# Kernel optimization log

Hardware: AMD Instinct MI355X
Metric: run time of the kernel (lower is better)

The kernel has to match this reference:

```python
import jax, jax.numpy as jnp
import numpy as np

D_MODEL = 1024
N_HEAD = 16


def setup_inputs() -> dict:
    key = jax.random.key(0)
    ks = jax.random.split(key, 9)
    d = D_MODEL
    s = 0.02
    return {
        "x": jax.random.normal(ks[0], (4, 2048, d), dtype=jnp.float32),
        "w_q": jax.random.normal(ks[1], (d, d), dtype=jnp.float32) * s,
        "b_q": jax.random.normal(ks[2], (d,), dtype=jnp.float32) * s,
        "w_k": jax.random.normal(ks[3], (d, d), dtype=jnp.float32) * s,
        "b_k": jax.random.normal(ks[4], (d,), dtype=jnp.float32) * s,
        "w_v": jax.random.normal(ks[5], (d, d), dtype=jnp.float32) * s,
        "b_v": jax.random.normal(ks[6], (d,), dtype=jnp.float32) * s,
        "w_o": jax.random.normal(ks[7], (d, d), dtype=jnp.float32) * s,
        "b_o": jax.random.normal(ks[8], (d,), dtype=jnp.float32) * s,
    }


def reference(x, w_q, b_q, w_k, b_k, w_v, b_v, w_o, b_o):
    B, S, D = x.shape
    H = N_HEAD
    dh = D // H

    def split(t):  # [B,S,D] -> [B,H,S,dh]
        return t.reshape(B, S, H, dh).transpose(0, 2, 1, 3)

    q = split(x @ w_q + b_q)
    k = split(x @ w_k + b_k)
    v = split(x @ w_v + b_v)

    scale = 1.0 / jnp.sqrt(jnp.float32(dh))
    score = jnp.einsum("bhqd,bhkd->bhqk", q, k) * scale
    score = jax.nn.softmax(score, axis=-1)
    out = jnp.einsum("bhqk,bhkd->bhqd", score, v)
    out = out.transpose(0, 2, 1, 3).reshape(B, S, D)
    return out @ w_o + b_o
```

## Files before the change

kernel.cpp:

```cpp
#include <hip/hip_runtime.h>


typedef __bf16 bf16x8 __attribute__((ext_vector_type(8)));
typedef float f32x4 __attribute__((ext_vector_type(4)));
typedef float f32x16 __attribute__((ext_vector_type(16)));
typedef unsigned short u16x8 __attribute__((ext_vector_type(8)));
typedef unsigned u32x4 __attribute__((ext_vector_type(4)));
typedef unsigned u32x2 __attribute__((ext_vector_type(2)));

#define SEQ 2048
#define DM 1024
#define NHEAD 16
#define MTOT 8192
#define QSCALE 0.18033688011112042f

__device__ __forceinline__ unsigned short f2bf(float f) {
  unsigned u = __builtin_bit_cast(unsigned, f);
  u += 0x7fffu + ((u >> 16) & 1u);
  return (unsigned short)(u >> 16);
}

__device__ __forceinline__ unsigned pkbf(float lo, float hi) {
  __bf16 a = (__bf16)lo, b = (__bf16)hi;
  return ((unsigned)__builtin_bit_cast(unsigned short, b) << 16) |
         __builtin_bit_cast(unsigned short, a);
}

__device__ __forceinline__ void async16(const void* g, void* l) {
  __builtin_amdgcn_global_load_lds(
      (const __attribute__((address_space(1))) void*)g,
      (__attribute__((address_space(3))) void*)l, 16, 0, 0);
}

template <bool CX>
__device__ __forceinline__ void exch(unsigned A, unsigned B, unsigned& fr0, unsigned& fr2) {
#if __has_builtin(__builtin_amdgcn_permlane32_swap)
  if constexpr (CX) {
    u32x2 r = __builtin_amdgcn_permlane32_swap(B, A, false, false);
    fr0 = r[1]; fr2 = r[0];
  } else {
    u32x2 r = __builtin_amdgcn_permlane32_swap(A, B, false, false);
    fr0 = r[0]; fr2 = r[1];
  }
#else
  int hi = (threadIdx.x & 63) >> 5;
  unsigned sA = (unsigned)__shfl_xor((int)A, 32);
  unsigned sB = (unsigned)__shfl_xor((int)B, 32);
  fr0 = hi ? sB : A;
  fr2 = hi ? B : sA;
#endif
}

__device__ __forceinline__ float halfsum(float rs) {
#if __has_builtin(__builtin_amdgcn_permlane32_swap)
  unsigned rb = __builtin_bit_cast(unsigned, rs);
  u32x2 rr = __builtin_amdgcn_permlane32_swap(rb, rb, false, false);
  return __builtin_bit_cast(float, rr[0]) + __builtin_bit_cast(float, rr[1]);
#else
  return rs + __shfl_xor(rs, 32);
#endif
}

__global__ __launch_bounds__(256) void k_cvt(const float* __restrict__ x,
                                             unsigned short* __restrict__ xb) {
  size_t i = ((size_t)blockIdx.x * 256 + threadIdx.x) * 8;
  float4 a = *(const float4*)(x + i);
  float4 b = *(const float4*)(x + i + 4);
  u16x8 o;
  o[0] = f2bf(a.x); o[1] = f2bf(a.y); o[2] = f2bf(a.z); o[3] = f2bf(a.w);
  o[4] = f2bf(b.x); o[5] = f2bf(b.y); o[6] = f2bf(b.z); o[7] = f2bf(b.w);
  *(u16x8*)(xb + i) = o;
}

__global__ __launch_bounds__(256) void k_wt(const float* __restrict__ w0, const float* __restrict__ w1,
                                            const float* __restrict__ w2, const float* __restrict__ w3,
                                            unsigned short* __restrict__ t0, unsigned short* __restrict__ t1,
                                            unsigned short* __restrict__ t2, unsigned short* __restrict__ t3) {
  __shared__ float t[64][65];
  int z = blockIdx.z;
  const float* w = z == 0 ? w0 : z == 1 ? w1 : z == 2 ? w2 : w3;
  unsigned short* wt = z == 0 ? t0 : z == 1 ? t1 : z == 2 ? t2 : t3;
  int nt = blockIdx.x, kt = blockIdx.y;
  int tx = threadIdx.x & 63, ty = threadIdx.x >> 6;
  for (int i = 0; i < 16; ++i) {
    int r = i * 4 + ty;
    t[r][tx] = w[(size_t)(kt * 64 + r) * DM + nt * 64 + tx];
  }
  __syncthreads();
  for (int i = 0; i < 16; ++i) {
    int r = i * 4 + ty;
    wt[(size_t)(nt * 64 + r) * DM + kt * 64 + tx] = f2bf(t[tx][r]);
  }
}

__device__ __forceinline__ void gemm_body(const unsigned short* __restrict__ A,
                                          const unsigned short* __restrict__ Bt,
                                          const float* __restrict__ bias,
                                          unsigned short* __restrict__ Cb,
                                          float* __restrict__ Cf, int bm, int bn, float sc) {
  __shared__ __align__(16) unsigned short As[128 * 64];
  __shared__ __align__(16) unsigned short Bs[128 * 64];
  const int K = DM, N = DM;
  int tid = threadIdx.x, w = tid >> 6, l = tid & 63;
  int g = l >> 4, l15 = l & 15;
  int wm = (w >> 1) * 64, wn = (w & 1) * 64;
  f32x4 acc[4][4];
#pragma unroll
  for (int mi = 0; mi < 4; ++mi)
#pragma unroll
    for (int ni = 0; ni < 4; ++ni)
#pragma unroll
      for (int e = 0; e < 4; ++e) acc[mi][ni][e] = 0.f;

  int lr8 = l >> 3, lp = l & 7;
  for (int kt = 0; kt < K / 64; ++kt) {
    __syncthreads();
#pragma unroll
    for (int i = 0; i < 4; ++i) {
      int cs = i * 4 + w;
      int row = cs * 8 + lr8;
      int c = lp ^ lr8;
      async16(A + (size_t)(bm + row) * K + kt * 64 + c * 8, &As[cs * 512]);
      async16(Bt + (size_t)(bn + row) * K + kt * 64 + c * 8, &Bs[cs * 512]);
    }
    __syncthreads();
    bf16x8 af[4][2];
#pragma unroll
    for (int mi = 0; mi < 4; ++mi)
#pragma unroll
      for (int kk = 0; kk < 2; ++kk) {
        int row = wm + mi * 16 + l15;
        af[mi][kk] = *(const bf16x8*)&As[row * 64 + (((kk * 4 + g) ^ (row & 7)) * 8)];
      }
    __builtin_amdgcn_s_setprio(1);
#pragma unroll
    for (int ni = 0; ni < 4; ++ni) {
      int row = wn + ni * 16 + l15;
      bf16x8 b0 = *(const bf16x8*)&Bs[row * 64 + (((0 + g) ^ (row & 7)) * 8)];
      bf16x8 b1 = *(const bf16x8*)&Bs[row * 64 + (((4 + g) ^ (row & 7)) * 8)];
#pragma unroll
      for (int mi = 0; mi < 4; ++mi) {
        acc[mi][ni] = __builtin_amdgcn_mfma_f32_16x16x32_bf16(af[mi][0], b0, acc[mi][ni], 0, 0, 0);
        acc[mi][ni] = __builtin_amdgcn_mfma_f32_16x16x32_bf16(af[mi][1], b1, acc[mi][ni], 0, 0, 0);
      }
    }
    __builtin_amdgcn_s_setprio(0);
  }
  float bv[4];
#pragma unroll
  for (int ni = 0; ni < 4; ++ni) bv[ni] = bias[bn + wn + ni * 16 + l15];
#pragma unroll
  for (int mi = 0; mi < 4; ++mi)
#pragma unroll
    for (int ni = 0; ni < 4; ++ni) {
      int col = bn + wn + ni * 16 + l15;
#pragma unroll
      for (int r = 0; r < 4; ++r) {
        int rowg = bm + wm + mi * 16 + g * 4 + r;
        float v = (acc[mi][ni][r] + bv[ni]) * sc;
        if (Cf) Cf[(size_t)rowg * N + col] = v;
        else    Cb[(size_t)rowg * N + col] = f2bf(v);
      }
    }
}

__global__ __launch_bounds__(256) void k_gemm(const unsigned short* __restrict__ A,
                                              const unsigned short* __restrict__ Bt,
                                              const float* __restrict__ bias,
                                              unsigned short* __restrict__ Cb,
                                              float* __restrict__ Cf) {
  gemm_body(A, Bt, bias, Cb, Cf, blockIdx.y * 128, blockIdx.x * 128, 1.f);
}

__global__ __launch_bounds__(256) void k_gemm_qkv(const unsigned short* __restrict__ A,
                                                  const unsigned short* bt0, const unsigned short* bt1,
                                                  const unsigned short* bt2,
                                                  const float* b0, const float* b1, const float* b2,
                                                  unsigned short* o0, unsigned short* o1,
                                                  unsigned short* o2) {
  int which = blockIdx.x >> 3;
  const unsigned short* Bt = which == 0 ? bt0 : which == 1 ? bt1 : bt2;
  const float* bias = which == 0 ? b0 : which == 1 ? b1 : b2;
  unsigned short* Cb = which == 0 ? o0 : which == 1 ? o1 : o2;
  float sc = which == 0 ? QSCALE : 1.f;
  gemm_body(A, Bt, bias, Cb, nullptr, blockIdx.y * 128, (blockIdx.x & 7) * 128, sc);
}

__global__ __launch_bounds__(256) void k_vt(const unsigned short* __restrict__ V,
                                            unsigned short* __restrict__ Vt) {
  __shared__ __align__(16) unsigned short t[64 * 64];
  int st = blockIdx.x, bh = blockIdx.y;
  int b = bh >> 4, h = bh & 15;
  int tid = threadIdx.x, w = tid >> 6, l = tid & 63;
  for (int i = 0; i < 2; ++i) {
    int cs = i * 4 + w;
    int row = cs * 8 + (l >> 3);
    int c = l & 7;
    async16(V + ((size_t)(b * SEQ + st * 64 + row) * DM + h * 64 + c * 8), &t[cs * 512]);
  }
  __syncthreads();
  for (int p = 0; p < 2; ++p) {
    int d = p * 32 + (tid >> 3);
    int cs = tid & 7;
    u16x8 o;
    for (int j = 0; j < 8; ++j) o[j] = t[(cs * 8 + j) * 64 + d];
    *(u16x8*)(Vt + ((size_t)bh * 64 + d) * SEQ + st * 64 + cs * 8) = o;
  }
}

template <bool CX>
__device__ __forceinline__ void attn_core(const unsigned short* __restrict__ Q,
                                          const unsigned short* __restrict__ Kg,
                                          const unsigned short* __restrict__ Vt,
                                          unsigned short* __restrict__ Og,
                                          unsigned short* smem, int b, int h, int bh, int qt) {
  int tid = threadIdx.x, w = tid >> 6, l = tid & 63;
  int l31 = l & 31, hi = l >> 5, l7 = l & 7;
  int lr8 = l >> 3, lp = l & 7;
  int q0w = qt * 128 + w * 32;
  unsigned short* const KS = smem;
  unsigned short* const VS = smem + 8192;

  bf16x8 qf[4];
#pragma unroll
  for (int c = 0; c < 4; ++c)
    qf[c] = *(const bf16x8*)(Q + (size_t)(b * SEQ + q0w + l31) * DM + h * 64 + c * 16 + hi * 8);

  const f32x16 fz = {0.f, 0.f, 0.f, 0.f, 0.f, 0.f, 0.f, 0.f,
                     0.f, 0.f, 0.f, 0.f, 0.f, 0.f, 0.f, 0.f};
  float lrow = 0.f;
  f32x16 oacc[2];
  oacc[0] = fz; oacc[1] = fz;

  auto stage = [&](int kt) {
    int s = kt & 1;
    unsigned short* kd = KS + s * 4096;
    unsigned short* vd = VS + s * 4096;
#pragma unroll
    for (int i = 0; i < 2; ++i) {
      int cs = i * 4 + w;
      int row = cs * 8 + lr8;
      int c = lp ^ lr8;
      async16(Kg + ((size_t)(b * SEQ + kt * 64 + row) * DM + h * 64 + c * 8), kd + cs * 512);
      async16(Vt + (((size_t)bh * 64 + row) * SEQ + kt * 64 + c * 8), vd + cs * 512);
    }
  };

  const int NT = SEQ / 64;
  stage(0);
  __syncthreads();
  for (int t = 0; t < NT; ++t) {
    int cur = t & 1;
    if (t + 1 < NT) stage(t + 1);
    const unsigned short* kc = KS + cur * 4096;
    const unsigned short* vc = VS + cur * 4096;

    f32x16 sacc[2];
    __builtin_amdgcn_s_setprio(1);
#pragma unroll
    for (int kh = 0; kh < 2; ++kh) {
      const unsigned short* kb = kc + (kh * 32 + l31) * 64;
      bf16x8 a0 = *(const bf16x8*)(kb + ((hi ^ l7) << 3));
      sacc[kh] = __builtin_amdgcn_mfma_f32_32x32x16_bf16(a0, qf[0], fz, 0, 0, 0);
#pragma unroll
      for (int c = 1; c < 4; ++c) {
        bf16x8 a = *(const bf16x8*)(kb + (((2 * c + hi) ^ l7) << 3));
        sacc[kh] = __builtin_amdgcn_mfma_f32_32x32x16_bf16(a, qf[c], sacc[kh], 0, 0, 0);
      }
    }
    __builtin_amdgcn_s_setprio(0);

    bf16x8 pf[4];
    {
      float r0 = 0.f, r1 = 0.f, r2 = 0.f, r3 = 0.f;
#pragma unroll
      for (int kh = 0; kh < 2; ++kh)
#pragma unroll
        for (int e = 0; e < 16; e += 4) {
          float p0 = __builtin_amdgcn_exp2f(sacc[kh][e + 0]);
          float p1 = __builtin_amdgcn_exp2f(sacc[kh][e + 1]);
          float p2 = __builtin_amdgcn_exp2f(sacc[kh][e + 2]);
          float p3 = __builtin_amdgcn_exp2f(sacc[kh][e + 3]);
          sacc[kh][e + 0] = p0; sacc[kh][e + 1] = p1;
          sacc[kh][e + 2] = p2; sacc[kh][e + 3] = p3;
          r0 += p0; r1 += p1; r2 += p2; r3 += p3;
        }
      lrow += halfsum((r0 + r1) + (r2 + r3));
#pragma unroll
      for (int ks = 0; ks < 4; ++ks) {
        int kh = ks >> 1, q4 = (ks & 1) * 8;
        unsigned A0 = pkbf(sacc[kh][q4 + 0], sacc[kh][q4 + 1]);
        unsigned A1 = pkbf(sacc[kh][q4 + 2], sacc[kh][q4 + 3]);
        unsigned B0 = pkbf(sacc[kh][q4 + 4], sacc[kh][q4 + 5]);
        unsigned B1 = pkbf(sacc[kh][q4 + 6], sacc[kh][q4 + 7]);
        unsigned f0, f1, f2, f3;
        exch<CX>(A0, B0, f0, f2);
        exch<CX>(A1, B1, f1, f3);
        u32x4 fr; fr[0] = f0; fr[1] = f1; fr[2] = f2; fr[3] = f3;
        pf[ks] = __builtin_bit_cast(bf16x8, fr);
      }
    }

    __builtin_amdgcn_s_setprio(1);
#pragma unroll
    for (int d = 0; d < 2; ++d) {
      const unsigned short* vb = vc + (d * 32 + l31) * 64;
#pragma unroll
      for (int ks = 0; ks < 4; ++ks) {
        bf16x8 a = *(const bf16x8*)(vb + (((2 * ks + hi) ^ l7) << 3));
        oacc[d] = __builtin_amdgcn_mfma_f32_32x32x16_bf16(a, pf[ks], oacc[d], 0, 0, 0);
      }
    }
    __builtin_amdgcn_s_setprio(0);
    __syncthreads();
  }

  float inv = 1.f / lrow;
  unsigned* ot = (unsigned*)smem + w * (32 * 33);
#pragma unroll
  for (int d = 0; d < 2; ++d)
#pragma unroll
    for (int qd = 0; qd < 4; ++qd) {
      unsigned u0 = pkbf(oacc[d][qd * 4 + 0] * inv, oacc[d][qd * 4 + 1] * inv);
      unsigned u1 = pkbf(oacc[d][qd * 4 + 2] * inv, oacc[d][qd * 4 + 3] * inv);
      int idx = l31 * 33 + d * 16 + qd * 4 + hi * 2;
      ot[idx] = u0;
      ot[idx + 1] = u1;
    }
  {
    int row = l >> 1, half = l & 1;
    const unsigned* sr = (const unsigned*)smem + w * (32 * 33) + row * 33 + half * 16;
    unsigned o[16];
#pragma unroll
    for (int j = 0; j < 16; ++j) o[j] = sr[j];
    size_t gbase = (size_t)(b * SEQ + q0w + row) * DM + h * 64 + half * 32;
#pragma unroll
    for (int i = 0; i < 4; ++i) {
      u32x4 t;
      t[0] = o[i * 4 + 0]; t[1] = o[i * 4 + 1]; t[2] = o[i * 4 + 2]; t[3] = o[i * 4 + 3];
      *(u32x4*)(Og + gbase + i * 8) = t;
    }
  }
}

__global__ __launch_bounds__(256, 4) void k_attn(const unsigned short* __restrict__ Q,
                                                 const unsigned short* __restrict__ Kg,
                                                 const unsigned short* __restrict__ Vt,
                                                 unsigned short* __restrict__ Og) {
  __shared__ __align__(16) unsigned short smem[16384];
  int bh = blockIdx.x, qt = blockIdx.y;
  int b = bh >> 4, h = bh & 15;
#if __has_builtin(__builtin_amdgcn_permlane32_swap)
  unsigned lid = threadIdx.x & 63;
  u32x2 pr = __builtin_amdgcn_permlane32_swap(lid, lid + 64u, false, false);
  bool convX = __builtin_amdgcn_readfirstlane(pr[0]) >= 64u;
#else
  bool convX = false;
#endif
  if (convX) attn_core<true>(Q, Kg, Vt, Og, smem, b, h, bh, qt);
  else       attn_core<false>(Q, Kg, Vt, Og, smem, b, h, bh, qt);
}

extern "C" void kernel_launch(void* const* d_in, const int* in_sizes, int n_in,
                              void* d_out, int out_size, void* d_ws, size_t ws_size,
                              hipStream_t stream) {
  const float* x  = (const float*)d_in[0];
  const float* wq = (const float*)d_in[1];
  const float* bq = (const float*)d_in[2];
  const float* wk = (const float*)d_in[3];
  const float* bk = (const float*)d_in[4];
  const float* wv = (const float*)d_in[5];
  const float* bv = (const float*)d_in[6];
  const float* wo = (const float*)d_in[7];
  const float* bo = (const float*)d_in[8];

  const size_t SZ_X = (size_t)MTOT * DM * 2;
  const size_t SZ_W = (size_t)DM * DM * 2;
  char* ws = (char*)d_ws;
  size_t off = 0;
  unsigned short* xb  = (unsigned short*)(ws + off); off += SZ_X;
  unsigned short* wqT = (unsigned short*)(ws + off); off += SZ_W;
  unsigned short* wkT = (unsigned short*)(ws + off); off += SZ_W;
  unsigned short* wvT = (unsigned short*)(ws + off); off += SZ_W;
  unsigned short* woT = (unsigned short*)(ws + off); off += SZ_W;
  unsigned short* Qb  = (unsigned short*)(ws + off); off += SZ_X;
  unsigned short* Kb  = (unsigned short*)(ws + off); off += SZ_X;
  unsigned short* Vb  = (unsigned short*)(ws + off); off += SZ_X;
  unsigned short* Vtb = (unsigned short*)(ws + off); off += SZ_X;
  unsigned short* Ab  = (unsigned short*)(ws + off); off += SZ_X;
  if (ws_size < off) return;

  k_cvt<<<dim3(4096), dim3(256), 0, stream>>>(x, xb);
  k_wt<<<dim3(16, 16, 4), dim3(256), 0, stream>>>(wq, wk, wv, wo, wqT, wkT, wvT, woT);
  k_gemm_qkv<<<dim3(24, 64), dim3(256), 0, stream>>>(xb, wqT, wkT, wvT, bq, bk, bv, Qb, Kb, Vb);
  k_vt<<<dim3(32, 64), dim3(256), 0, stream>>>(Vb, Vtb);
  k_attn<<<dim3(64, 16), dim3(256), 0, stream>>>(Qb, Kb, Vtb, Ab);
  k_gemm<<<dim3(8, 64), dim3(256), 0, stream>>>(Ab, woT, bo, nullptr, (float*)d_out);
}
```

Measured before the change: 185.2 us.

## Fuse V transpose into QKV GEMM epilogue and remap block order per XCD

```diff
diff --git a/kernel.cpp b/kernel.cpp
--- a/kernel.cpp
+++ b/kernel.cpp
@@ -5,6 +5,7 @@
 typedef float f32x4 __attribute__((ext_vector_type(4)));
 typedef float f32x16 __attribute__((ext_vector_type(16)));
 typedef unsigned short u16x8 __attribute__((ext_vector_type(8)));
+typedef unsigned short u16x4 __attribute__((ext_vector_type(4)));
 typedef unsigned u32x4 __attribute__((ext_vector_type(4)));
 typedef unsigned u32x2 __attribute__((ext_vector_type(2)));
 
@@ -97,9 +98,12 @@
                                           const unsigned short* __restrict__ Bt,
                                           const float* __restrict__ bias,
                                           unsigned short* __restrict__ Cb,
-                                          float* __restrict__ Cf, int bm, int bn, float sc) {
-  __shared__ __align__(16) unsigned short As[128 * 64];
-  __shared__ __align__(16) unsigned short Bs[128 * 64];
+                                          float* __restrict__ Cf,
+                                          unsigned short* __restrict__ Vt,
+                                          int bm, int bn, float sc) {
+  __shared__ __align__(16) unsigned short sh[16384];
+  unsigned short* const As = sh;
+  unsigned short* const Bs = sh + 8192;
   const int K = DM, N = DM;
   int tid = threadIdx.x, w = tid >> 6, l = tid & 63;
   int g = l >> 4, l15 = l & 15;
@@ -149,6 +153,40 @@
   float bv[4];
 #pragma unroll
   for (int ni = 0; ni < 4; ++ni) bv[ni] = bias[bn + wn + ni * 16 + l15];
+
+  if (Vt) {
+    __syncthreads();
+#pragma unroll
+    for (int mi = 0; mi < 4; ++mi)
+#pragma unroll
+      for (int ni = 0; ni < 4; ++ni) {
+        int nl = wn + ni * 16 + l15;
+        int sl = wm + mi * 16 + g * 4;
+        u16x4 pk;
+#pragma unroll
+        for (int r = 0; r < 4; ++r) pk[r] = f2bf((acc[mi][ni][r] + bv[ni]) * sc);
+        *(u16x4*)&sh[nl * 128 + (sl ^ ((nl & 7) << 3))] = pk;
+      }
+    __syncthreads();
+    {
+      int nl = tid >> 1, s0 = (tid & 1) * 64;
+      int xs = (nl & 7) << 3;
+      bf16x8 grp[8];
+#pragma unroll
+      for (int m = 0; m < 8; ++m)
+        grp[m ^ (xs >> 3)] = *(const bf16x8*)&sh[nl * 128 + s0 + 8 * m];
+      int coln = bn + nl;
+      int hh = (coln >> 6) & 15, dd = coln & 63;
+      int bb = bm >> 11;
+      int sg = (bm & 2047) + s0;
+      unsigned short* dst = Vt + ((size_t)((bb * NHEAD + hh) * 64 + dd)) * SEQ + sg;
+#pragma unroll
+      for (int m = 0; m < 8; ++m)
+        *(u16x8*)(dst + 8 * m) = __builtin_bit_cast(u16x8, grp[m]);
+    }
+    return;
+  }
+
 #pragma unroll
   for (int mi = 0; mi < 4; ++mi)
 #pragma unroll
@@ -169,7 +207,10 @@
                                               const float* __restrict__ bias,
                                               unsigned short* __restrict__ Cb,
                                               float* __restrict__ Cf) {
-  gemm_body(A, Bt, bias, Cb, Cf, blockIdx.y * 128, blockIdx.x * 128, 1.f);
+  int L = blockIdx.x + blockIdx.y * 8;
+  int Lp = (L & 7) * 64 + (L >> 3);
+  int bx = Lp & 7, by = Lp >> 3;
+  gemm_body(A, Bt, bias, Cb, Cf, nullptr, by * 128, bx * 128, 1.f);
 }
 
 __global__ __launch_bounds__(256) void k_gemm_qkv(const unsigned short* __restrict__ A,
@@ -177,35 +218,17 @@
                                                   const unsigned short* bt2,
                                                   const float* b0, const float* b1, const float* b2,
                                                   unsigned short* o0, unsigned short* o1,
-                                                  unsigned short* o2) {
-  int which = blockIdx.x >> 3;
+                                                  unsigned short* vt) {
+  int L = blockIdx.x + blockIdx.y * 24;
+  int Lp = (L & 7) * 192 + (L >> 3);
+  int bx = Lp % 24, by = Lp / 24;
+  int which = bx >> 3;
   const unsigned short* Bt = which == 0 ? bt0 : which == 1 ? bt1 : bt2;
   const float* bias = which == 0 ? b0 : which == 1 ? b1 : b2;
-  unsigned short* Cb = which == 0 ? o0 : which == 1 ? o1 : o2;
+  unsigned short* Cb = which == 0 ? o0 : which == 1 ? o1 : nullptr;
+  unsigned short* Vt = which == 2 ? vt : nullptr;
   float sc = which == 0 ? QSCALE : 1.f;
-  gemm_body(A, Bt, bias, Cb, nullptr, blockIdx.y * 128, (blockIdx.x & 7) * 128, sc);
-}
-
-__global__ __launch_bounds__(256) void k_vt(const unsigned short* __restrict__ V,
-                                            unsigned short* __restrict__ Vt) {
-  __shared__ __align__(16) unsigned short t[64 * 64];
-  int st = blockIdx.x, bh = blockIdx.y;
-  int b = bh >> 4, h = bh & 15;
-  int tid = threadIdx.x, w = tid >> 6, l = tid & 63;
-  for (int i = 0; i < 2; ++i) {
-    int cs = i * 4 + w;
-    int row = cs * 8 + (l >> 3);
-    int c = l & 7;
-    async16(V + ((size_t)(b * SEQ + st * 64 + row) * DM + h * 64 + c * 8), &t[cs * 512]);
-  }
-  __syncthreads();
-  for (int p = 0; p < 2; ++p) {
-    int d = p * 32 + (tid >> 3);
-    int cs = tid & 7;
-    u16x8 o;
-    for (int j = 0; j < 8; ++j) o[j] = t[(cs * 8 + j) * 64 + d];
-    *(u16x8*)(Vt + ((size_t)bh * 64 + d) * SEQ + st * 64 + cs * 8) = o;
-  }
+  gemm_body(A, Bt, bias, Cb, nullptr, Vt, by * 128, (bx & 7) * 128, sc);
 }
 
 template <bool CX>
@@ -385,15 +408,13 @@
   unsigned short* woT = (unsigned short*)(ws + off); off += SZ_W;
   unsigned short* Qb  = (unsigned short*)(ws + off); off += SZ_X;
   unsigned short* Kb  = (unsigned short*)(ws + off); off += SZ_X;
-  unsigned short* Vb  = (unsigned short*)(ws + off); off += SZ_X;
   unsigned short* Vtb = (unsigned short*)(ws + off); off += SZ_X;
   unsigned short* Ab  = (unsigned short*)(ws + off); off += SZ_X;
   if (ws_size < off) return;
 
   k_cvt<<<dim3(4096), dim3(256), 0, stream>>>(x, xb);
   k_wt<<<dim3(16, 16, 4), dim3(256), 0, stream>>>(wq, wk, wv, wo, wqT, wkT, wvT, woT);
-  k_gemm_qkv<<<dim3(24, 64), dim3(256), 0, stream>>>(xb, wqT, wkT, wvT, bq, bk, bv, Qb, Kb, Vb);
-  k_vt<<<dim3(32, 64), dim3(256), 0, stream>>>(Vb, Vtb);
+  k_gemm_qkv<<<dim3(24, 64), dim3(256), 0, stream>>>(xb, wqT, wkT, wvT, bq, bk, bv, Qb, Kb, Vtb);
   k_attn<<<dim3(64, 16), dim3(256), 0, stream>>>(Qb, Kb, Vtb, Ab);
   k_gemm<<<dim3(8, 64), dim3(256), 0, stream>>>(Ab, woT, bo, nullptr, (float*)d_out);
 }
```

Measured after the change: 237.4 us. 1.28x slower.
